# Optimization experiments

Measured on AMD Instinct MI355X. Metric: run time of the kernel, lower is better.

The kernel has to match this reference:

```python
import jax, jax.numpy as jnp
import numpy as np

IN_FEATURES = 4096
OUT_FEATURES = 4096
RANK = 64


def setup_inputs() -> dict:
    key = jax.random.key(0)
    ks = jax.random.split(key, 8)
    # target stddev from module init: sqrt(1/(in+out)); spread across 6 cores
    target_sdv = np.sqrt(1.0 / (IN_FEATURES + OUT_FEATURES))
    core_scale = np.float32(target_sdv ** (1.0 / 6.0))
    x = jax.random.normal(ks[0], (4, 2048, IN_FEATURES), dtype=jnp.float32)
    f0 = jax.random.normal(ks[1], (1, 16, RANK), dtype=jnp.float32) * core_scale
    f1 = jax.random.normal(ks[2], (RANK, 16, RANK), dtype=jnp.float32) * core_scale
    f2 = jax.random.normal(ks[3], (RANK, 16, RANK), dtype=jnp.float32) * core_scale
    f3 = jax.random.normal(ks[4], (RANK, 16, RANK), dtype=jnp.float32) * core_scale
    f4 = jax.random.normal(ks[5], (RANK, 16, RANK), dtype=jnp.float32) * core_scale
    f5 = jax.random.normal(ks[6], (RANK, 16, 1), dtype=jnp.float32) * core_scale
    stdv = np.float32(1.0 / np.sqrt(OUT_FEATURES))
    bias = jax.random.uniform(ks[7], (OUT_FEATURES,), dtype=jnp.float32,
                              minval=-stdv, maxval=stdv)
    return {"x": x, "f0": f0, "f1": f1, "f2": f2, "f3": f3,
            "f4": f4, "f5": f5, "bias": bias}


def reference(x, f0, f1, f2, f3, f4, f5, bias):
    # forward_tt_full_precision: chain tensordot over TT cores, reshape, GEMM.
    W = f0  # [1, 16, r]
    for U in (f1, f2, f3, f4, f5):
        W = jnp.tensordot(W, U, axes=[[-1], [0]])
    # W: [1,16,16,16,16,16,16,1] -> [in_features, out_features]
    W = W.reshape(IN_FEATURES, OUT_FEATURES)
    return x @ W + bias
```

## Files before the change

kernel.cpp:

```cpp
#include <hip/hip_runtime.h>

#define IN_F 4096
#define OUT_F 4096
#define NROWS 8192

typedef __attribute__((ext_vector_type(8))) short short8;
typedef __attribute__((ext_vector_type(4))) float f32x4;
typedef unsigned short ushort_t;

__device__ __forceinline__ ushort_t bf_hi(float v) {
  return (ushort_t)(__float_as_uint(v) >> 16);
}
__device__ __forceinline__ ushort_t bf_lo(float v) {
  float h = __uint_as_float(__float_as_uint(v) & 0xFFFF0000u);
  return (ushort_t)(__float_as_uint(v - h) >> 16);
}

__global__ __launch_bounds__(256) void tt_p1(
    const float* __restrict__ f0, const float* __restrict__ f1,
    const float* __restrict__ f4, const float* __restrict__ f5,
    float* __restrict__ G, float* __restrict__ H) {
  int g = blockIdx.x * 256 + threadIdx.x;
  if (g < 16384) {
    int i12 = g >> 6, r2 = g & 63;
    int i1 = i12 >> 4, i2 = i12 & 15;
    const float* a = f0 + i1 * 64;
    const float* b = f1 + i2 * 64 + r2;
    float s = 0.f;
#pragma unroll
    for (int r1 = 0; r1 < 64; ++r1) s += a[r1] * b[r1 * 1024];
    G[g] = s;
  } else {
    int h = g - 16384;
    int r4 = h >> 8, i56 = h & 255;
    int i5 = i56 >> 4, i6 = i56 & 15;
    const float* a = f4 + r4 * 1024 + i5 * 64;
    const float* b = f5 + i6;
    float s = 0.f;
#pragma unroll
    for (int r5 = 0; r5 < 64; ++r5) s += a[r5] * b[r5 * 16];
    H[h] = s;
  }
}

__global__ __launch_bounds__(256) void tt_p2(
    const float* __restrict__ f2, const float* __restrict__ f3,
    const float* __restrict__ G, const float* __restrict__ H,
    ushort_t* __restrict__ LT_hi, ushort_t* __restrict__ LT_lo,
    ushort_t* __restrict__ RT_hi, ushort_t* __restrict__ RT_lo) {
  int g = blockIdx.x * 256 + threadIdx.x;
  if (g < 262144) {
    int r3 = g >> 12, row = g & 4095;
    int i12 = row >> 4, i3 = row & 15;
    const float* a = G + i12 * 64;
    const float* b = f2 + i3 * 64 + r3;
    float s = 0.f;
#pragma unroll
    for (int r2 = 0; r2 < 64; ++r2) s += a[r2] * b[r2 * 1024];
    LT_hi[g] = bf_hi(s);
    LT_lo[g] = bf_lo(s);
  } else {
    int h = g - 262144;
    int col = h >> 6, r3 = h & 63;
    int i4 = col >> 8, i56 = col & 255;
    const float* a = f3 + r3 * 1024 + i4 * 64;
    const float* b = H + i56;
    float s = 0.f;
#pragma unroll
    for (int r4 = 0; r4 < 64; ++r4) s += a[r4] * b[r4 * 256];
    RT_hi[h] = bf_hi(s);
    RT_lo[h] = bf_lo(s);
  }
}

__global__ __launch_bounds__(256) void tt_xl(
    const float* __restrict__ x, const ushort_t* __restrict__ LT_hi,
    const ushort_t* __restrict__ LT_lo, float* __restrict__ tpart, int KC) {
  int tid = threadIdx.x;
  int lane = tid & 63, w = tid >> 6;
  int lr = lane & 15, lk = lane >> 4;
  long rb0 = (long)blockIdx.x * 128 + w * 32;
  int k0 = blockIdx.y * KC;
  int nks = KC >> 5;

  f32x4 acc[2][4] = {};

  for (int ks = 0; ks < nks; ++ks) {
    int ka = k0 + ks * 32 + lk * 8;
    short8 ahi[2], alo[2];
#pragma unroll
    for (int m = 0; m < 2; ++m) {
      const float* xp = x + (rb0 + 16 * m + lr) * IN_F + ka;
      float4 v0 = *reinterpret_cast<const float4*>(xp);
      float4 v1 = *reinterpret_cast<const float4*>(xp + 4);
      float vv[8] = {v0.x, v0.y, v0.z, v0.w, v1.x, v1.y, v1.z, v1.w};
#pragma unroll
      for (int j = 0; j < 8; ++j) {
        ahi[m][j] = (short)bf_hi(vv[j]);
        alo[m][j] = (short)bf_lo(vv[j]);
      }
    }
#pragma unroll
    for (int n = 0; n < 4; ++n) {
      int col = 16 * n + lr;
      short8 bhi = *reinterpret_cast<const short8*>(LT_hi + (size_t)col * 4096 + ka);
      short8 blo = *reinterpret_cast<const short8*>(LT_lo + (size_t)col * 4096 + ka);
#pragma unroll
      for (int m = 0; m < 2; ++m) {
        acc[m][n] = __builtin_amdgcn_mfma_f32_16x16x32_bf16(ahi[m], bhi, acc[m][n], 0, 0, 0);
        acc[m][n] = __builtin_amdgcn_mfma_f32_16x16x32_bf16(ahi[m], blo, acc[m][n], 0, 0, 0);
        acc[m][n] = __builtin_amdgcn_mfma_f32_16x16x32_bf16(alo[m], bhi, acc[m][n], 0, 0, 0);
      }
    }
  }

  float* op = tpart + (size_t)blockIdx.y * ((size_t)NROWS * 64);
#pragma unroll
  for (int m = 0; m < 2; ++m)
#pragma unroll
    for (int n = 0; n < 4; ++n)
#pragma unroll
      for (int r = 0; r < 4; ++r) {
        long row = rb0 + 16 * m + 4 * lk + r;
        op[row * 64 + 16 * n + lr] = acc[m][n][r];
      }
}

__global__ __launch_bounds__(256) void tt_red(
    const float* __restrict__ tpart, ushort_t* __restrict__ t_hi,
    ushort_t* __restrict__ t_lo, int splitk) {
  int g = blockIdx.x * 256 + threadIdx.x;
  float4 s = make_float4(0.f, 0.f, 0.f, 0.f);
  const float4* p = reinterpret_cast<const float4*>(tpart) + g;
  for (int i = 0; i < splitk; ++i) {
    float4 v = p[(size_t)i * (NROWS * 16)];
    s.x += v.x; s.y += v.y; s.z += v.z; s.w += v.w;
  }
  float vv[4] = {s.x, s.y, s.z, s.w};
  ushort4 hv, lv;
  hv.x = bf_hi(vv[0]); hv.y = bf_hi(vv[1]); hv.z = bf_hi(vv[2]); hv.w = bf_hi(vv[3]);
  lv.x = bf_lo(vv[0]); lv.y = bf_lo(vv[1]); lv.z = bf_lo(vv[2]); lv.w = bf_lo(vv[3]);
  *reinterpret_cast<ushort4*>(t_hi + (size_t)g * 4) = hv;
  *reinterpret_cast<ushort4*>(t_lo + (size_t)g * 4) = lv;
}

__global__ __launch_bounds__(256) void tt_tr(
    const ushort_t* __restrict__ t_hi, const ushort_t* __restrict__ t_lo,
    const ushort_t* __restrict__ RT_hi, const ushort_t* __restrict__ RT_lo,
    const float* __restrict__ bias, float* __restrict__ y) {
  int tid = threadIdx.x;
  int lane = tid & 63, w = tid >> 6;
  int lr = lane & 15, lk = lane >> 4;
  long rb0 = (long)blockIdx.y * 64;
  int cb0 = blockIdx.x * 256 + w * 64;

  f32x4 acc[4][4] = {};

#pragma unroll
  for (int ks = 0; ks < 2; ++ks) {
    int ka = ks * 32 + lk * 8;
    short8 ahi[4], alo[4];
#pragma unroll
    for (int m = 0; m < 4; ++m) {
      size_t off = (size_t)(rb0 + 16 * m + lr) * 64 + ka;
      ahi[m] = *reinterpret_cast<const short8*>(t_hi + off);
      alo[m] = *reinterpret_cast<const short8*>(t_lo + off);
    }
#pragma unroll
    for (int n = 0; n < 4; ++n) {
      size_t off = (size_t)(cb0 + 16 * n + lr) * 64 + ka;
      short8 bhi = *reinterpret_cast<const short8*>(RT_hi + off);
      short8 blo = *reinterpret_cast<const short8*>(RT_lo + off);
#pragma unroll
      for (int m = 0; m < 4; ++m) {
        acc[m][n] = __builtin_amdgcn_mfma_f32_16x16x32_bf16(ahi[m], bhi, acc[m][n], 0, 0, 0);
        acc[m][n] = __builtin_amdgcn_mfma_f32_16x16x32_bf16(ahi[m], blo, acc[m][n], 0, 0, 0);
        acc[m][n] = __builtin_amdgcn_mfma_f32_16x16x32_bf16(alo[m], bhi, acc[m][n], 0, 0, 0);
      }
    }
  }

#pragma unroll
  for (int n = 0; n < 4; ++n) {
    float bv = bias[cb0 + 16 * n + lr];
#pragma unroll
    for (int m = 0; m < 4; ++m)
#pragma unroll
      for (int r = 0; r < 4; ++r) {
        long row = rb0 + 16 * m + 4 * lk + r;
        y[row * (long)OUT_F + cb0 + 16 * n + lr] = acc[m][n][r] + bv;
      }
  }
}

extern "C" void kernel_launch(void* const* d_in, const int* in_sizes, int n_in,
                              void* d_out, int out_size, void* d_ws,
                              size_t ws_size, hipStream_t stream) {
  (void)in_sizes; (void)n_in; (void)out_size;
  const float* x    = (const float*)d_in[0];
  const float* f0   = (const float*)d_in[1];
  const float* f1   = (const float*)d_in[2];
  const float* f2   = (const float*)d_in[3];
  const float* f3   = (const float*)d_in[4];
  const float* f4   = (const float*)d_in[5];
  const float* f5   = (const float*)d_in[6];
  const float* bias = (const float*)d_in[7];
  float* y = (float*)d_out;

  float* G = (float*)d_ws;
  float* H = G + 16384;
  ushort_t* LT_hi = (ushort_t*)(H + 16384);
  ushort_t* LT_lo = LT_hi + 262144;
  ushort_t* RT_hi = LT_lo + 262144;
  ushort_t* RT_lo = RT_hi + 262144;
  ushort_t* t_hi  = RT_lo + 262144;
  ushort_t* t_lo  = t_hi + 524288;
  float* tpart = (float*)(t_lo + 524288);

  int splitk = 16;
  while (splitk > 1 &&
         (size_t)4325376 + (size_t)splitk * 2097152 > ws_size)
    splitk >>= 1;
  int KC = 4096 / splitk;

  tt_p1<<<128, 256, 0, stream>>>(f0, f1, f4, f5, G, H);
  tt_p2<<<2048, 256, 0, stream>>>(f2, f3, G, H, LT_hi, LT_lo, RT_hi, RT_lo);
  tt_xl<<<dim3(64, splitk), 256, 0, stream>>>(x, LT_hi, LT_lo, tpart, KC);
  tt_red<<<512, 256, 0, stream>>>(tpart, t_hi, t_lo, splitk);
  tt_tr<<<dim3(16, 128), 256, 0, stream>>>(t_hi, t_lo, RT_hi, RT_lo, bias, y);
}
```

Baseline: 354.1 us.

## Interleave LT hi/lo into k-blocked layout and prefetch x one step ahead

tt_p2 now writes the left TT factor as a single interleaved buffer blocked by 8 k-values, with the hi and lo bf16 halves stored next to each other, so each tt_xl lane loads a contiguous 32-byte chunk instead of two strided 16-byte loads. Thread indexing in tt_p2 is also swapped so that both the LT and RT stores get the new ordering. tt_xl software-prefetches the next k-step of x into registers before issuing the MFMAs and batches all B loads ahead of the compute. This raises register pressure and produces scattered stores in tt_p2.

```diff
diff --git a/kernel.cpp b/kernel.cpp
--- a/kernel.cpp
+++ b/kernel.cpp
@@ -46,36 +46,37 @@
 __global__ __launch_bounds__(256) void tt_p2(
     const float* __restrict__ f2, const float* __restrict__ f3,
     const float* __restrict__ G, const float* __restrict__ H,
-    ushort_t* __restrict__ LT_hi, ushort_t* __restrict__ LT_lo,
+    ushort_t* __restrict__ LT2,
     ushort_t* __restrict__ RT_hi, ushort_t* __restrict__ RT_lo) {
   int g = blockIdx.x * 256 + threadIdx.x;
   if (g < 262144) {
-    int r3 = g >> 12, row = g & 4095;
+    int r3 = g & 63, row = g >> 6;
     int i12 = row >> 4, i3 = row & 15;
     const float* a = G + i12 * 64;
     const float* b = f2 + i3 * 64 + r3;
     float s = 0.f;
 #pragma unroll
     for (int r2 = 0; r2 < 64; ++r2) s += a[r2] * b[r2 * 1024];
-    LT_hi[g] = bf_hi(s);
-    LT_lo[g] = bf_lo(s);
+    ushort_t* p = LT2 + ((size_t)((row >> 3) * 64 + r3) * 16 + (row & 7));
+    p[0] = bf_hi(s);
+    p[8] = bf_lo(s);
   } else {
     int h = g - 262144;
-    int col = h >> 6, r3 = h & 63;
+    int r3 = h >> 12, col = h & 4095;
     int i4 = col >> 8, i56 = col & 255;
     const float* a = f3 + r3 * 1024 + i4 * 64;
     const float* b = H + i56;
     float s = 0.f;
 #pragma unroll
     for (int r4 = 0; r4 < 64; ++r4) s += a[r4] * b[r4 * 256];
-    RT_hi[h] = bf_hi(s);
-    RT_lo[h] = bf_lo(s);
+    RT_hi[(size_t)col * 64 + r3] = bf_hi(s);
+    RT_lo[(size_t)col * 64 + r3] = bf_lo(s);
   }
 }
 
 __global__ __launch_bounds__(256) void tt_xl(
-    const float* __restrict__ x, const ushort_t* __restrict__ LT_hi,
-    const ushort_t* __restrict__ LT_lo, float* __restrict__ tpart, int KC) {
+    const float* __restrict__ x, const ushort_t* __restrict__ LT2,
+    float* __restrict__ tpart, int KC) {
   int tid = threadIdx.x;
   int lane = tid & 63, w = tid >> 6;
   int lr = lane & 15, lk = lane >> 4;
@@ -84,34 +85,52 @@
   int nks = KC >> 5;
 
   f32x4 acc[2][4] = {};
+  float4 xr[2][2];
+
+#pragma unroll
+  for (int m = 0; m < 2; ++m) {
+    const float* xp = x + (rb0 + 16 * m + lr) * IN_F + k0 + lk * 8;
+    xr[m][0] = *reinterpret_cast<const float4*>(xp);
+    xr[m][1] = *reinterpret_cast<const float4*>(xp + 4);
+  }
 
   for (int ks = 0; ks < nks; ++ks) {
-    int ka = k0 + ks * 32 + lk * 8;
     short8 ahi[2], alo[2];
 #pragma unroll
     for (int m = 0; m < 2; ++m) {
-      const float* xp = x + (rb0 + 16 * m + lr) * IN_F + ka;
-      float4 v0 = *reinterpret_cast<const float4*>(xp);
-      float4 v1 = *reinterpret_cast<const float4*>(xp + 4);
-      float vv[8] = {v0.x, v0.y, v0.z, v0.w, v1.x, v1.y, v1.z, v1.w};
+      float vv[8] = {xr[m][0].x, xr[m][0].y, xr[m][0].z, xr[m][0].w,
+                     xr[m][1].x, xr[m][1].y, xr[m][1].z, xr[m][1].w};
 #pragma unroll
       for (int j = 0; j < 8; ++j) {
         ahi[m][j] = (short)bf_hi(vv[j]);
         alo[m][j] = (short)bf_lo(vv[j]);
       }
     }
+    int kb = (k0 >> 3) + ks * 4 + lk;
+    short8 bhi[4], blo[4];
 #pragma unroll
     for (int n = 0; n < 4; ++n) {
-      int col = 16 * n + lr;
-      short8 bhi = *reinterpret_cast<const short8*>(LT_hi + (size_t)col * 4096 + ka);
-      short8 blo = *reinterpret_cast<const short8*>(LT_lo + (size_t)col * 4096 + ka);
+      const ushort_t* bp = LT2 + ((size_t)kb * 64 + 16 * n + lr) * 16;
+      bhi[n] = *reinterpret_cast<const short8*>(bp);
+      blo[n] = *reinterpret_cast<const short8*>(bp + 8);
+    }
+    if (ks + 1 < nks) {
 #pragma unroll
       for (int m = 0; m < 2; ++m) {
-        acc[m][n] = __builtin_amdgcn_mfma_f32_16x16x32_bf16(ahi[m], bhi, acc[m][n], 0, 0, 0);
-        acc[m][n] = __builtin_amdgcn_mfma_f32_16x16x32_bf16(ahi[m], blo, acc[m][n], 0, 0, 0);
-        acc[m][n] = __builtin_amdgcn_mfma_f32_16x16x32_bf16(alo[m], bhi, acc[m][n], 0, 0, 0);
-      }
-    }
+        const float* xp =
+            x + (rb0 + 16 * m + lr) * IN_F + k0 + (ks + 1) * 32 + lk * 8;
+        xr[m][0] = *reinterpret_cast<const float4*>(xp);
+        xr[m][1] = *reinterpret_cast<const float4*>(xp + 4);
+      }
+    }
+#pragma unroll
+    for (int n = 0; n < 4; ++n)
+#pragma unroll
+      for (int m = 0; m < 2; ++m) {
+        acc[m][n] = __builtin_amdgcn_mfma_f32_16x16x32_bf16(ahi[m], bhi[n], acc[m][n], 0, 0, 0);
+        acc[m][n] = __builtin_amdgcn_mfma_f32_16x16x32_bf16(ahi[m], blo[n], acc[m][n], 0, 0, 0);
+        acc[m][n] = __builtin_amdgcn_mfma_f32_16x16x32_bf16(alo[m], bhi[n], acc[m][n], 0, 0, 0);
+      }
   }
 
   float* op = tpart + (size_t)blockIdx.y * ((size_t)NROWS * 64);
@@ -209,9 +228,8 @@
 
   float* G = (float*)d_ws;
   float* H = G + 16384;
-  ushort_t* LT_hi = (ushort_t*)(H + 16384);
-  ushort_t* LT_lo = LT_hi + 262144;
-  ushort_t* RT_hi = LT_lo + 262144;
+  ushort_t* LT2   = (ushort_t*)(H + 16384);
+  ushort_t* RT_hi = LT2 + 524288;
   ushort_t* RT_lo = RT_hi + 262144;
   ushort_t* t_hi  = RT_lo + 262144;
   ushort_t* t_lo  = t_hi + 524288;
@@ -224,8 +242,8 @@
   int KC = 4096 / splitk;
 
   tt_p1<<<128, 256, 0, stream>>>(f0, f1, f4, f5, G, H);
-  tt_p2<<<2048, 256, 0, stream>>>(f2, f3, G, H, LT_hi, LT_lo, RT_hi, RT_lo);
-  tt_xl<<<dim3(64, splitk), 256, 0, stream>>>(x, LT_hi, LT_lo, tpart, KC);
+  tt_p2<<<2048, 256, 0, stream>>>(f2, f3, G, H, LT2, RT_hi, RT_lo);
+  tt_xl<<<dim3(64, splitk), 256, 0, stream>>>(x, LT2, tpart, KC);
   tt_red<<<512, 256, 0, stream>>>(tpart, t_hi, t_lo, splitk);
   tt_tr<<<dim3(16, 128), 256, 0, stream>>>(t_hi, t_lo, RT_hi, RT_lo, bias, y);
 }
```

New measurement: 322.1 us. -9.0%, faster.
